# Kernel optimization log

Measured on AMD Instinct MI355X. Metric: run time of the kernel, lower is better.

The kernel has to match this reference:

```python
import jax, jax.numpy as jnp
import numpy as np

N, CS, CZ, CH, H, PQK, PV = 768, 384, 128, 16, 12, 4, 8
INF, EPS = 1e5, 1e-8


def setup_inputs() -> dict:
    key = jax.random.key(0)
    ks = jax.random.split(key, 12)
    w = lambda k, i, o: (jax.random.normal(k, (i, o), jnp.float32) * 0.02)
    inp = {
        's': jax.random.normal(ks[0], (N, CS), jnp.float32),
        'z': jax.random.normal(ks[1], (N, N, CZ), jnp.float32),
        'rot': jax.random.normal(ks[2], (N, 3, 3), jnp.float32),
        'trans': jax.random.normal(ks[3], (N, 3), jnp.float32),
        'mask': jnp.ones((N,), jnp.float32),
        'W_q': w(ks[4], CS, H * CH), 'b_q': jnp.zeros((H * CH,), jnp.float32),
        'W_kv': w(ks[5], CS, 2 * H * CH), 'b_kv': jnp.zeros((2 * H * CH,), jnp.float32),
        'W_qp': w(ks[6], CS, H * PQK * 3), 'b_qp': jnp.zeros((H * PQK * 3,), jnp.float32),
        'W_kvp': w(ks[7], CS, H * (PQK + PV) * 3), 'b_kvp': jnp.zeros((H * (PQK + PV) * 3,), jnp.float32),
        'W_b': w(ks[8], CZ, H), 'b_b': jnp.zeros((H,), jnp.float32),
        'head_weights': jnp.full((H,), 0.541324854612918, jnp.float32),  # softplus^-1(1)
        'W_out': w(ks[9], H * (CZ + CH + PV * 4), CS), 'b_out': jnp.zeros((CS,), jnp.float32),
    }
    return inp


def reference(s, z, rot, trans, mask, W_q, b_q, W_kv, b_kv, W_qp, b_qp, W_kvp, b_kvp,
              W_b, b_b, head_weights, W_out, b_out):
    n = s.shape[0]
    # scalar q/k/v
    q = (s @ W_q + b_q).reshape(n, H, CH)
    kv = (s @ W_kv + b_kv).reshape(n, H, 2 * CH)
    k, v = kv[..., :CH], kv[..., CH:]

    def make_points(W, b, P):
        p = (s @ W + b).reshape(n, 3, H * P)         # 3 contiguous coord chunks (x,y,z)
        p = jnp.transpose(p, (0, 2, 1))              # [n, H*P, 3]
        p = jnp.einsum('nij,npj->npi', rot, p) + trans[:, None, :]  # global frame
        return p.reshape(n, H, P, 3)

    q_pts = make_points(W_qp, b_qp, PQK)
    kv_pts = make_points(W_kvp, b_kvp, PQK + PV)
    k_pts, v_pts = kv_pts[:, :, :PQK], kv_pts[:, :, PQK:]

    b_pair = z @ W_b + b_b                                       # [n, n, H]
    a = jnp.einsum('qhc,khc->hqk', q, k) * np.sqrt(1.0 / (3 * CH))
    a = a + np.sqrt(1.0 / 3) * jnp.transpose(b_pair, (2, 0, 1))

    # point-distance attention term
    d2 = jnp.sum((q_pts[:, None] - k_pts[None]) ** 2, axis=-1)   # [q, k, H, Pqk]
    hw = jax.nn.softplus(head_weights) * np.sqrt(1.0 / (3 * (PQK * 9.0 / 2)))
    pt_att = -0.5 * jnp.sum(d2 * hw[None, None, :, None], axis=-1)  # [q, k, H]
    a = a + jnp.transpose(pt_att, (2, 0, 1))

    sq_mask = INF * (mask[:, None] * mask[None, :] - 1.0)
    a = jax.nn.softmax(a + sq_mask[None], axis=-1)               # [H, q, k]

    o = jnp.einsum('hqk,khc->qhc', a, v).reshape(n, H * CH)
    o_pt = jnp.einsum('hqk,khpc->qhpc', a, v_pts)                # [q, H, Pv, 3]
    o_pt = jnp.einsum('nba,nhpb->nhpa', rot, o_pt - trans[:, None, None, :])  # invert_apply
    o_pt_norm = jnp.sqrt(jnp.sum(o_pt ** 2, axis=-1) + EPS).reshape(n, H * PV)
    o_pt_flat = o_pt.reshape(n, H * PV, 3)
    o_pair = jnp.einsum('hqk,qkc->qhc', a, z).reshape(n, H * CZ)

    cat = jnp.concatenate([o, o_pt_flat[..., 0], o_pt_flat[..., 1], o_pt_flat[..., 2],
                           o_pt_norm, o_pair], axis=-1)          # [n, H*(CZ+CH+Pv*4)]
    return cat @ W_out + b_out
```

## Files before the change

kernel.cpp:

```cpp
#include <hip/hip_runtime.h>
#include <hip/hip_bf16.h>
#include <math.h>

#define NRES 768
#define CS   384
#define CZ   128
#define CH   16
#define NH   12
#define PQK  4
#define PV   8
#define QCOLS   (NH*CH)
#define KVCOLS  (2*NH*CH)
#define QPCOLS  (NH*PQK*3)
#define KVPCOLS (NH*(PQK+PV)*3)
#define CATC    (NH*(CZ+CH+PV*4))
#define NN      (NRES*NRES)

__global__ __launch_bounds__(256) void proj_kernel(
    const float* __restrict__ s,
    const float* __restrict__ Wq,  const float* __restrict__ bq,
    const float* __restrict__ Wkv, const float* __restrict__ bkv,
    const float* __restrict__ Wqp, const float* __restrict__ bqp,
    const float* __restrict__ Wkvp,const float* __restrict__ bkvp,
    float* __restrict__ proj_q, float* __restrict__ proj_kv,
    float* __restrict__ proj_qp, float* __restrict__ proj_kvp)
{
    __shared__ float Al[32][68];
    __shared__ float Bl[32][52];
    const int mt = blockIdx.x;
    const int gc0 = blockIdx.y * 48;
    const float* W; const float* bb; int ncol; float* dst; int c0;
    if (gc0 < 192)      { W=Wq;   bb=bq;   ncol=QCOLS;   dst=proj_q;   c0=gc0; }
    else if (gc0 < 576) { W=Wkv;  bb=bkv;  ncol=KVCOLS;  dst=proj_kv;  c0=gc0-192; }
    else if (gc0 < 720) { W=Wqp;  bb=bqp;  ncol=QPCOLS;  dst=proj_qp;  c0=gc0-576; }
    else                { W=Wkvp; bb=bkvp; ncol=KVPCOLS; dst=proj_kvp; c0=gc0-720; }
    const int tid = threadIdx.x;
    const int m0 = (tid & 15)*4;
    const int n0 = (tid >> 4)*3;
    float acc[4][3] = {};
    for (int kc = 0; kc < CS; kc += 32) {
        #pragma unroll
        for (int f = tid; f < 512; f += 256) {
            int r = f >> 3, c4 = (f & 7)*4;
            float4 v = *(const float4*)(s + (size_t)(mt*64+r)*CS + kc + c4);
            Al[c4][r]=v.x; Al[c4+1][r]=v.y; Al[c4+2][r]=v.z; Al[c4+3][r]=v.w;
        }
        for (int f = tid; f < 384; f += 256) {
            int r = f / 12, c4 = (f % 12)*4;
            *(float4*)&Bl[r][c4] = *(const float4*)(W + (size_t)(kc+r)*ncol + c0 + c4);
        }
        __syncthreads();
        #pragma unroll
        for (int kk = 0; kk < 32; ++kk) {
            float4 a = *(const float4*)&Al[kk][m0];
            float b0 = Bl[kk][n0], b1 = Bl[kk][n0+1], b2 = Bl[kk][n0+2];
            acc[0][0]+=a.x*b0; acc[0][1]+=a.x*b1; acc[0][2]+=a.x*b2;
            acc[1][0]+=a.y*b0; acc[1][1]+=a.y*b1; acc[1][2]+=a.y*b2;
            acc[2][0]+=a.z*b0; acc[2][1]+=a.z*b1; acc[2][2]+=a.z*b2;
            acc[3][0]+=a.w*b0; acc[3][1]+=a.w*b1; acc[3][2]+=a.w*b2;
        }
        __syncthreads();
    }
    #pragma unroll
    for (int r = 0; r < 4; ++r)
        #pragma unroll
        for (int c = 0; c < 3; ++c)
            dst[(size_t)(mt*64+m0+r)*ncol + c0+n0+c] = acc[r][c] + bb[c0+n0+c];
}

__global__ __launch_bounds__(256) void rotpts_kernel(
    const float* __restrict__ rot, const float* __restrict__ trans,
    const float* __restrict__ proj_q, const float* __restrict__ proj_kv,
    const float* __restrict__ proj_qp, const float* __restrict__ proj_kvp,
    const float* __restrict__ b_out,
    float* __restrict__ qfrag, float* __restrict__ kcat, float* __restrict__ vcatT,
    float* __restrict__ out)
{
    int g = blockIdx.x*256 + threadIdx.x;
    const int S0 = NRES*48;
    const int S1 = S0 + NRES*432;
    const int S2 = S1 + NRES*192;
    const int S3 = S2 + NRES*384;
    const int S4 = S3 + NRES*CS;
    if (g < S0) {
        int n = g/48, rem = g%48;
        int h = rem>>2, p = rem&3;
        float p0 = proj_qp[(size_t)n*QPCOLS + rem];
        float p1 = proj_qp[(size_t)n*QPCOLS + 48 + rem];
        float p2 = proj_qp[(size_t)n*QPCOLS + 96 + rem];
        const float* Rm = rot + (size_t)n*9; const float* t = trans + (size_t)n*3;
        float* dq = qfrag + ((size_t)n*12 + h)*28 + 16 + p*3;
        #pragma unroll
        for (int i = 0; i < 3; ++i)
            dq[i] = Rm[i*3]*p0 + Rm[i*3+1]*p1 + Rm[i*3+2]*p2 + t[i];
    } else if (g < S1) {
        int g2 = g - S0;
        int n = g2 % 768, t = g2 / 768;
        int h = t/36, u = t%36, p = u/3, i = u%3;
        int col = h*12 + p;
        float p0 = proj_kvp[(size_t)n*KVPCOLS + col];
        float p1 = proj_kvp[(size_t)n*KVPCOLS + 144 + col];
        float p2 = proj_kvp[(size_t)n*KVPCOLS + 288 + col];
        float val = rot[(size_t)n*9 + i*3]*p0 + rot[(size_t)n*9 + i*3+1]*p1
                  + rot[(size_t)n*9 + i*3+2]*p2 + trans[(size_t)n*3 + i];
        if (p < PQK) kcat[(size_t)(h*28 + 16 + p*3 + i)*NRES + n] = val;
        else         vcatT[(size_t)(h*40 + 16 + (p-4)*3 + i)*NRES + n] = val;
    } else if (g < S2) {
        int g3 = g - S1;
        int n = g3 / 192, c = g3 % 192;
        int h = c >> 4, cc = c & 15;
        qfrag[((size_t)n*12 + h)*28 + cc] = proj_q[(size_t)n*QCOLS + c];
    } else if (g < S3) {
        int g4 = g - S2;
        int n = g4 % 768, col = g4 / 768;
        int h = col >> 5, cc = col & 31;
        float val = proj_kv[(size_t)n*KVCOLS + col];
        if (cc < 16) kcat[(size_t)(h*28 + cc)*NRES + n] = val;
        else         vcatT[(size_t)(h*40 + (cc-16))*NRES + n] = val;
    } else if (g < S4) {
        int g5 = g - S3;
        out[g5] = b_out[g5 % CS];
    }
}

__global__ __launch_bounds__(256) void bias_kernel(
    const float* __restrict__ z, const float* __restrict__ mask,
    const float* __restrict__ W_b, const float* __restrict__ b_b,
    float* __restrict__ lg)
{
    int r = blockIdx.x*256 + threadIdx.x;
    int q = r / 768, k = r - q*768;
    const float4* zr = (const float4*)(z + (size_t)r*CZ);
    float acc[12] = {};
    #pragma unroll
    for (int c4 = 0; c4 < 32; ++c4) {
        float4 v = zr[c4];
        const float* w0 = W_b + c4*48;
        #pragma unroll
        for (int h = 0; h < 12; ++h)
            acc[h] += v.x*w0[h] + v.y*w0[12+h] + v.z*w0[24+h] + v.w*w0[36+h];
    }
    float mterm = 100000.0f*(mask[q]*mask[k] - 1.0f);
    const float scale_b = 0.5773502691896258f;
    #pragma unroll
    for (int h = 0; h < 12; ++h)
        lg[(size_t)h*NN + r] = scale_b*(acc[h] + b_b[h]) + mterm;
}

__global__ __launch_bounds__(256) void softmax_fused_kernel(
    float* __restrict__ lg, const float* __restrict__ qfrag, const float* __restrict__ kcat,
    const float* __restrict__ head_w, const float* __restrict__ vcatT,
    float* __restrict__ cat, float* __restrict__ optt)
{
    const int h = blockIdx.x % 12;
    const int q = (blockIdx.x / 12)*4 + (threadIdx.x >> 6);
    const int ln = threadIdx.x & 63;
    const float scale_qk = 0.14433756729740643f;
    float x = head_w[h];
    float sp = (x > 20.f) ? x : log1pf(__expf(x));
    float coef = -0.5f * sp * 0.13608276348795434f;

    float qf[28];
    const float* qp = qfrag + ((size_t)q*12 + h)*28;
    #pragma unroll
    for (int c = 0; c < 28; ++c) qf[c] = qp[c];

    float* arow = lg + (size_t)h*NN + (size_t)q*NRES;
    const float* kb = kcat + (size_t)h*28*NRES;
    float4 a[3];
    #pragma unroll
    for (int i = 0; i < 3; ++i) {
        a[i] = *(const float4*)(arow + ln*4 + i*256);
        float4 d = {0.f,0.f,0.f,0.f}, p2 = {0.f,0.f,0.f,0.f};
        #pragma unroll
        for (int c = 0; c < 16; ++c) {
            float4 kv = *(const float4*)(kb + (size_t)c*NRES + ln*4 + i*256);
            d.x += qf[c]*kv.x; d.y += qf[c]*kv.y; d.z += qf[c]*kv.z; d.w += qf[c]*kv.w;
        }
        #pragma unroll
        for (int c = 16; c < 28; ++c) {
            float4 kv = *(const float4*)(kb + (size_t)c*NRES + ln*4 + i*256);
            float t0 = qf[c]-kv.x, t1 = qf[c]-kv.y, t2 = qf[c]-kv.z, t3 = qf[c]-kv.w;
            p2.x += t0*t0; p2.y += t1*t1; p2.z += t2*t2; p2.w += t3*t3;
        }
        a[i].x += scale_qk*d.x + coef*p2.x;
        a[i].y += scale_qk*d.y + coef*p2.y;
        a[i].z += scale_qk*d.z + coef*p2.z;
        a[i].w += scale_qk*d.w + coef*p2.w;
    }
    float m = -1e30f;
    #pragma unroll
    for (int i=0;i<3;++i) m = fmaxf(m, fmaxf(fmaxf(a[i].x,a[i].y),fmaxf(a[i].z,a[i].w)));
    #pragma unroll
    for (int o=32;o>0;o>>=1) m = fmaxf(m, __shfl_xor(m,o,64));
    float ssum = 0.f;
    #pragma unroll
    for (int i=0;i<3;++i) {
        a[i].x = __expf(a[i].x-m); a[i].y = __expf(a[i].y-m);
        a[i].z = __expf(a[i].z-m); a[i].w = __expf(a[i].w-m);
        ssum += a[i].x + a[i].y + a[i].z + a[i].w;
    }
    #pragma unroll
    for (int o=32;o>0;o>>=1) ssum += __shfl_xor(ssum,o,64);
    float inv = 1.f/ssum;
    #pragma unroll
    for (int i=0;i<3;++i) {
        a[i].x*=inv; a[i].y*=inv; a[i].z*=inv; a[i].w*=inv;
        *(float4*)(arow + ln*4 + i*256) = a[i];
    }
    for (int col = 0; col < 40; ++col) {
        const float* vrow = vcatT + (size_t)(h*40+col)*NRES;
        float p = 0.f;
        #pragma unroll
        for (int i=0;i<3;++i) {
            float4 v = *(const float4*)(vrow + ln*4 + i*256);
            p += a[i].x*v.x + a[i].y*v.y + a[i].z*v.z + a[i].w*v.w;
        }
        #pragma unroll
        for (int o=32;o>0;o>>=1) p += __shfl_xor(p,o,64);
        if (ln == 0) {
            if (col < 16) cat[(size_t)q*CATC + h*16 + col] = p;
            else          optt[(size_t)q*288 + h*24 + (col-16)] = p;
        }
    }
}

__global__ __launch_bounds__(256, 2) void opair_kernel(
    const float* __restrict__ z, const float* __restrict__ lg,
    const float* __restrict__ rot, const float* __restrict__ trans,
    const float* __restrict__ optt, float* __restrict__ cat)
{
    __shared__ float abuf[12][768];
    __shared__ float obuf[12][132];
    const int q = blockIdx.x, tid = threadIdx.x;
    float* crow = cat + (size_t)q*CATC;

    for (int f = tid; f < 2304; f += 256) {
        int hh = f / 192, k4 = f % 192;
        *(float4*)&abuf[hh][k4*4] = *(const float4*)(lg + (size_t)hh*NN + (size_t)q*NRES + (size_t)k4*4);
    }
    for (int f = tid; f < 12*132; f += 256) ((float*)obuf)[f] = 0.f;
    __syncthreads();

    if (tid < 96) {
        int hh = tid>>3, p = tid&7;
        float b0 = optt[(size_t)q*288 + hh*24+p*3+0] - trans[q*3+0];
        float b1 = optt[(size_t)q*288 + hh*24+p*3+1] - trans[q*3+1];
        float b2 = optt[(size_t)q*288 + hh*24+p*3+2] - trans[q*3+2];
        const float* Rm = rot + (size_t)q*9;
        float v0 = Rm[0]*b0 + Rm[3]*b1 + Rm[6]*b2;
        float v1 = Rm[1]*b0 + Rm[4]*b1 + Rm[7]*b2;
        float v2 = Rm[2]*b0 + Rm[5]*b1 + Rm[8]*b2;
        crow[192 + tid] = v0;
        crow[288 + tid] = v1;
        crow[384 + tid] = v2;
        crow[480 + tid] = sqrtf(v0*v0 + v1*v1 + v2*v2 + 1e-8f);
    }

    const int c4 = (tid & 31)*4;
    const int kg = tid >> 5;
    const float* zq = z + (size_t)q*NRES*CZ + c4;
    float4 acc[12];
    #pragma unroll
    for (int h = 0; h < 12; ++h) acc[h] = make_float4(0.f,0.f,0.f,0.f);
    const int k0 = kg*96;
    #pragma unroll 4
    for (int k = k0; k < k0+96; ++k) {
        float4 zv = *(const float4*)(zq + (size_t)k*CZ);
        #pragma unroll
        for (int h = 0; h < 12; ++h) {
            float aw = abuf[h][k];
            acc[h].x += aw*zv.x; acc[h].y += aw*zv.y;
            acc[h].z += aw*zv.z; acc[h].w += aw*zv.w;
        }
    }
    for (int g = 0; g < 8; ++g) {
        __syncthreads();
        if (kg == g) {
            #pragma unroll
            for (int h = 0; h < 12; ++h) {
                obuf[h][c4+0] += acc[h].x; obuf[h][c4+1] += acc[h].y;
                obuf[h][c4+2] += acc[h].z; obuf[h][c4+3] += acc[h].w;
            }
        }
    }
    __syncthreads();
    for (int f = tid; f < 384; f += 256) {
        int h = f >> 5, cc4 = (f & 31)*4;
        float4 o = *(const float4*)&obuf[h][cc4];
        *(float4*)(crow + 576 + h*128 + cc4) = o;
    }
}

__global__ __launch_bounds__(256) void outgemm_kernel(
    const float* __restrict__ cat, const float* __restrict__ W_out,
    float* __restrict__ out)
{
    __shared__ float Al[32][68];
    __shared__ float Bl[32][68];
    const int mt = blockIdx.x;
    const int nt = blockIdx.y;
    const int kt = blockIdx.z;
    const int tid = threadIdx.x;
    const int m0 = (tid & 15)*4, n0 = (tid >> 4)*4;
    float acc[4][4] = {};
    for (int ki = 0; ki < 11; ++ki) {
        int kc = kt*352 + ki*32;
        #pragma unroll
        for (int f = tid; f < 512; f += 256) {
            int r = f >> 3, c4 = (f & 7)*4;
            float4 v = *(const float4*)(cat + (size_t)(mt*64+r)*CATC + kc + c4);
            Al[c4][r]=v.x; Al[c4+1][r]=v.y; Al[c4+2][r]=v.z; Al[c4+3][r]=v.w;
        }
        #pragma unroll
        for (int f = tid; f < 512; f += 256) {
            int r = f >> 4, c4 = (f & 15)*4;
            *(float4*)&Bl[r][c4] = *(const float4*)(W_out + (size_t)(kc+r)*CS + nt*64 + c4);
        }
        __syncthreads();
        #pragma unroll
        for (int kk = 0; kk < 32; ++kk) {
            float4 a = *(const float4*)&Al[kk][m0];
            float4 b = *(const float4*)&Bl[kk][n0];
            acc[0][0]+=a.x*b.x; acc[0][1]+=a.x*b.y; acc[0][2]+=a.x*b.z; acc[0][3]+=a.x*b.w;
            acc[1][0]+=a.y*b.x; acc[1][1]+=a.y*b.y; acc[1][2]+=a.y*b.z; acc[1][3]+=a.y*b.w;
            acc[2][0]+=a.z*b.x; acc[2][1]+=a.z*b.y; acc[2][2]+=a.z*b.z; acc[2][3]+=a.z*b.w;
            acc[3][0]+=a.w*b.x; acc[3][1]+=a.w*b.y; acc[3][2]+=a.w*b.z; acc[3][3]+=a.w*b.w;
        }
        __syncthreads();
    }
    #pragma unroll
    for (int r = 0; r < 4; ++r)
        #pragma unroll
        for (int c = 0; c < 4; ++c)
            atomicAdd(&out[(size_t)(mt*64+m0+r)*CS + nt*64+n0+c], acc[r][c]);
}

extern "C" void kernel_launch(void* const* d_in, const int* in_sizes, int n_in,
                              void* d_out, int out_size, void* d_ws, size_t ws_size,
                              hipStream_t stream) {
    const float* s      = (const float*)d_in[0];
    const float* z      = (const float*)d_in[1];
    const float* rot    = (const float*)d_in[2];
    const float* trans  = (const float*)d_in[3];
    const float* mask   = (const float*)d_in[4];
    const float* W_q    = (const float*)d_in[5];
    const float* b_q    = (const float*)d_in[6];
    const float* W_kv   = (const float*)d_in[7];
    const float* b_kv   = (const float*)d_in[8];
    const float* W_qp   = (const float*)d_in[9];
    const float* b_qp   = (const float*)d_in[10];
    const float* W_kvp  = (const float*)d_in[11];
    const float* b_kvp  = (const float*)d_in[12];
    const float* W_b    = (const float*)d_in[13];
    const float* b_b    = (const float*)d_in[14];
    const float* head_w = (const float*)d_in[15];
    const float* W_out  = (const float*)d_in[16];
    const float* b_out  = (const float*)d_in[17];

    float* ws = (float*)d_ws;
    float* lg       = ws;
    float* proj_q   = ws;
    float* proj_kv  = ws + 147456;
    float* proj_qp  = ws + 442368;
    float* proj_kvp = ws + 552960;
    float* vcatT    = ws + 7077888;
    float* qfrag    = ws + 7446528;
    float* kcat     = ws + 7704576;
    float* optt     = ws + 7962624;
    float* cat      = ws + 8183808;
    float* out = (float*)d_out;

    proj_kernel<<<dim3(12,24), 256, 0, stream>>>(s, W_q, b_q, W_kv, b_kv, W_qp, b_qp, W_kvp, b_kvp,
                                                 proj_q, proj_kv, proj_qp, proj_kvp);
    rotpts_kernel<<<4320, 256, 0, stream>>>(rot, trans, proj_q, proj_kv, proj_qp, proj_kvp, b_out,
                                            qfrag, kcat, vcatT, out);
    bias_kernel<<<NN/256, 256, 0, stream>>>(z, mask, W_b, b_b, lg);
    softmax_fused_kernel<<<12*(NRES/4), 256, 0, stream>>>(lg, qfrag, kcat, head_w, vcatT, cat, optt);
    opair_kernel<<<NRES, 256, 0, stream>>>(z, lg, rot, trans, optt, cat);
    outgemm_kernel<<<dim3(12,6,6), 256, 0, stream>>>(cat, W_out, out);
}
```

Baseline: 727.9 us.

## Fuse softmax/PV kernel into pair-output kernel, keep attention in shared memory

Merges the softmax-plus-value-projection kernel with the z-weighted pair aggregation kernel, so each block handles one query row across all 12 heads. Normalized attention rows are written straight into shared memory instead of going to global memory and being read back, and point outputs stay in a small shared buffer instead of a global scratch array. This removes one launch and a full write plus reread of the 12x768x768 attention tensor. In exchange each wave runs the softmax for three heads in sequence, leaving fewer blocks (768) and less parallelism in that phase. Occupancy is pinned with a launch bound of 3 blocks per unit.

```diff
diff --git a/kernel.cpp b/kernel.cpp
--- a/kernel.cpp
+++ b/kernel.cpp
@@ -147,106 +147,100 @@
         lg[(size_t)h*NN + r] = scale_b*(acc[h] + b_b[h]) + mterm;
 }
 
-__global__ __launch_bounds__(256) void softmax_fused_kernel(
-    float* __restrict__ lg, const float* __restrict__ qfrag, const float* __restrict__ kcat,
+__global__ __launch_bounds__(256, 3) void smpv_kernel(
+    const float* __restrict__ z, const float* __restrict__ lg,
+    const float* __restrict__ qfrag, const float* __restrict__ kcat,
     const float* __restrict__ head_w, const float* __restrict__ vcatT,
-    float* __restrict__ cat, float* __restrict__ optt)
-{
-    const int h = blockIdx.x % 12;
-    const int q = (blockIdx.x / 12)*4 + (threadIdx.x >> 6);
-    const int ln = threadIdx.x & 63;
-    const float scale_qk = 0.14433756729740643f;
-    float x = head_w[h];
-    float sp = (x > 20.f) ? x : log1pf(__expf(x));
-    float coef = -0.5f * sp * 0.13608276348795434f;
-
-    float qf[28];
-    const float* qp = qfrag + ((size_t)q*12 + h)*28;
-    #pragma unroll
-    for (int c = 0; c < 28; ++c) qf[c] = qp[c];
-
-    float* arow = lg + (size_t)h*NN + (size_t)q*NRES;
-    const float* kb = kcat + (size_t)h*28*NRES;
-    float4 a[3];
-    #pragma unroll
-    for (int i = 0; i < 3; ++i) {
-        a[i] = *(const float4*)(arow + ln*4 + i*256);
-        float4 d = {0.f,0.f,0.f,0.f}, p2 = {0.f,0.f,0.f,0.f};
-        #pragma unroll
-        for (int c = 0; c < 16; ++c) {
-            float4 kv = *(const float4*)(kb + (size_t)c*NRES + ln*4 + i*256);
-            d.x += qf[c]*kv.x; d.y += qf[c]*kv.y; d.z += qf[c]*kv.z; d.w += qf[c]*kv.w;
-        }
-        #pragma unroll
-        for (int c = 16; c < 28; ++c) {
-            float4 kv = *(const float4*)(kb + (size_t)c*NRES + ln*4 + i*256);
-            float t0 = qf[c]-kv.x, t1 = qf[c]-kv.y, t2 = qf[c]-kv.z, t3 = qf[c]-kv.w;
-            p2.x += t0*t0; p2.y += t1*t1; p2.z += t2*t2; p2.w += t3*t3;
-        }
-        a[i].x += scale_qk*d.x + coef*p2.x;
-        a[i].y += scale_qk*d.y + coef*p2.y;
-        a[i].z += scale_qk*d.z + coef*p2.z;
-        a[i].w += scale_qk*d.w + coef*p2.w;
-    }
-    float m = -1e30f;
-    #pragma unroll
-    for (int i=0;i<3;++i) m = fmaxf(m, fmaxf(fmaxf(a[i].x,a[i].y),fmaxf(a[i].z,a[i].w)));
-    #pragma unroll
-    for (int o=32;o>0;o>>=1) m = fmaxf(m, __shfl_xor(m,o,64));
-    float ssum = 0.f;
-    #pragma unroll
-    for (int i=0;i<3;++i) {
-        a[i].x = __expf(a[i].x-m); a[i].y = __expf(a[i].y-m);
-        a[i].z = __expf(a[i].z-m); a[i].w = __expf(a[i].w-m);
-        ssum += a[i].x + a[i].y + a[i].z + a[i].w;
-    }
-    #pragma unroll
-    for (int o=32;o>0;o>>=1) ssum += __shfl_xor(ssum,o,64);
-    float inv = 1.f/ssum;
-    #pragma unroll
-    for (int i=0;i<3;++i) {
-        a[i].x*=inv; a[i].y*=inv; a[i].z*=inv; a[i].w*=inv;
-        *(float4*)(arow + ln*4 + i*256) = a[i];
-    }
-    for (int col = 0; col < 40; ++col) {
-        const float* vrow = vcatT + (size_t)(h*40+col)*NRES;
-        float p = 0.f;
-        #pragma unroll
-        for (int i=0;i<3;++i) {
-            float4 v = *(const float4*)(vrow + ln*4 + i*256);
-            p += a[i].x*v.x + a[i].y*v.y + a[i].z*v.z + a[i].w*v.w;
-        }
-        #pragma unroll
-        for (int o=32;o>0;o>>=1) p += __shfl_xor(p,o,64);
-        if (ln == 0) {
-            if (col < 16) cat[(size_t)q*CATC + h*16 + col] = p;
-            else          optt[(size_t)q*288 + h*24 + (col-16)] = p;
-        }
-    }
-}
-
-__global__ __launch_bounds__(256, 2) void opair_kernel(
-    const float* __restrict__ z, const float* __restrict__ lg,
     const float* __restrict__ rot, const float* __restrict__ trans,
-    const float* __restrict__ optt, float* __restrict__ cat)
+    float* __restrict__ cat)
 {
     __shared__ float abuf[12][768];
     __shared__ float obuf[12][132];
+    __shared__ float optl[12][24];
     const int q = blockIdx.x, tid = threadIdx.x;
+    const int w = tid >> 6, ln = tid & 63;
     float* crow = cat + (size_t)q*CATC;
-
-    for (int f = tid; f < 2304; f += 256) {
-        int hh = f / 192, k4 = f % 192;
-        *(float4*)&abuf[hh][k4*4] = *(const float4*)(lg + (size_t)hh*NN + (size_t)q*NRES + (size_t)k4*4);
-    }
+    const float scale_qk = 0.14433756729740643f;
+
     for (int f = tid; f < 12*132; f += 256) ((float*)obuf)[f] = 0.f;
+
+    for (int hh = 0; hh < 3; ++hh) {
+        const int h = w*3 + hh;
+        float x = head_w[h];
+        float sp = (x > 20.f) ? x : log1pf(__expf(x));
+        float coef = -0.5f * sp * 0.13608276348795434f;
+
+        float qf[28];
+        const float* qp = qfrag + ((size_t)q*12 + h)*28;
+        #pragma unroll
+        for (int c = 0; c < 28; ++c) qf[c] = qp[c];
+
+        const float* arow = lg + (size_t)h*NN + (size_t)q*NRES;
+        const float* kb = kcat + (size_t)h*28*NRES;
+        float4 a[3];
+        #pragma unroll
+        for (int i = 0; i < 3; ++i) {
+            a[i] = *(const float4*)(arow + ln*4 + i*256);
+            float4 d = {0.f,0.f,0.f,0.f}, p2 = {0.f,0.f,0.f,0.f};
+            #pragma unroll
+            for (int c = 0; c < 16; ++c) {
+                float4 kv = *(const float4*)(kb + (size_t)c*NRES + ln*4 + i*256);
+                d.x += qf[c]*kv.x; d.y += qf[c]*kv.y; d.z += qf[c]*kv.z; d.w += qf[c]*kv.w;
+            }
+            #pragma unroll
+            for (int c = 16; c < 28; ++c) {
+                float4 kv = *(const float4*)(kb + (size_t)c*NRES + ln*4 + i*256);
+                float t0 = qf[c]-kv.x, t1 = qf[c]-kv.y, t2 = qf[c]-kv.z, t3 = qf[c]-kv.w;
+                p2.x += t0*t0; p2.y += t1*t1; p2.z += t2*t2; p2.w += t3*t3;
+            }
+            a[i].x += scale_qk*d.x + coef*p2.x;
+            a[i].y += scale_qk*d.y + coef*p2.y;
+            a[i].z += scale_qk*d.z + coef*p2.z;
+            a[i].w += scale_qk*d.w + coef*p2.w;
+        }
+        float m = -1e30f;
+        #pragma unroll
+        for (int i=0;i<3;++i) m = fmaxf(m, fmaxf(fmaxf(a[i].x,a[i].y),fmaxf(a[i].z,a[i].w)));
+        #pragma unroll
+        for (int o=32;o>0;o>>=1) m = fmaxf(m, __shfl_xor(m,o,64));
+        float ssum = 0.f;
+        #pragma unroll
+        for (int i=0;i<3;++i) {
+            a[i].x = __expf(a[i].x-m); a[i].y = __expf(a[i].y-m);
+            a[i].z = __expf(a[i].z-m); a[i].w = __expf(a[i].w-m);
+            ssum += a[i].x + a[i].y + a[i].z + a[i].w;
+        }
+        #pragma unroll
+        for (int o=32;o>0;o>>=1) ssum += __shfl_xor(ssum,o,64);
+        float inv = 1.f/ssum;
+        #pragma unroll
+        for (int i=0;i<3;++i) {
+            a[i].x*=inv; a[i].y*=inv; a[i].z*=inv; a[i].w*=inv;
+            *(float4*)&abuf[h][ln*4 + i*256] = a[i];
+        }
+        for (int col = 0; col < 40; ++col) {
+            const float* vrow = vcatT + (size_t)(h*40+col)*NRES;
+            float p = 0.f;
+            #pragma unroll
+            for (int i=0;i<3;++i) {
+                float4 v = *(const float4*)(vrow + ln*4 + i*256);
+                p += a[i].x*v.x + a[i].y*v.y + a[i].z*v.z + a[i].w*v.w;
+            }
+            #pragma unroll
+            for (int o=32;o>0;o>>=1) p += __shfl_xor(p,o,64);
+            if (ln == 0) {
+                if (col < 16) crow[h*16 + col] = p;
+                else          optl[h][col-16] = p;
+            }
+        }
+    }
     __syncthreads();
 
     if (tid < 96) {
         int hh = tid>>3, p = tid&7;
-        float b0 = optt[(size_t)q*288 + hh*24+p*3+0] - trans[q*3+0];
-        float b1 = optt[(size_t)q*288 + hh*24+p*3+1] - trans[q*3+1];
-        float b2 = optt[(size_t)q*288 + hh*24+p*3+2] - trans[q*3+2];
+        float b0 = optl[hh][p*3+0] - trans[q*3+0];
+        float b1 = optl[hh][p*3+1] - trans[q*3+1];
+        float b2 = optl[hh][p*3+2] - trans[q*3+2];
         const float* Rm = rot + (size_t)q*9;
         float v0 = Rm[0]*b0 + Rm[3]*b1 + Rm[6]*b2;
         float v1 = Rm[1]*b0 + Rm[4]*b1 + Rm[7]*b2;
@@ -367,8 +361,7 @@
     float* vcatT    = ws + 7077888;
     float* qfrag    = ws + 7446528;
     float* kcat     = ws + 7704576;
-    float* optt     = ws + 7962624;
-    float* cat      = ws + 8183808;
+    float* cat      = ws + 7962624;
     float* out = (float*)d_out;
 
     proj_kernel<<<dim3(12,24), 256, 0, stream>>>(s, W_q, b_q, W_kv, b_kv, W_qp, b_qp, W_kvp, b_kvp,
@@ -376,7 +369,6 @@
     rotpts_kernel<<<4320, 256, 0, stream>>>(rot, trans, proj_q, proj_kv, proj_qp, proj_kvp, b_out,
                                             qfrag, kcat, vcatT, out);
     bias_kernel<<<NN/256, 256, 0, stream>>>(z, mask, W_b, b_b, lg);
-    softmax_fused_kernel<<<12*(NRES/4), 256, 0, stream>>>(lg, qfrag, kcat, head_w, vcatT, cat, optt);
-    opair_kernel<<<NRES, 256, 0, stream>>>(z, lg, rot, trans, optt, cat);
+    smpv_kernel<<<NRES, 256, 0, stream>>>(z, lg, qfrag, kcat, head_w, vcatT, rot, trans, cat);
     outgemm_kernel<<<dim3(12,6,6), 256, 0, stream>>>(cat, W_out, out);
 }
```

After: 919.0 us. 26.3% more time.
